# Kernel optimization log

Measured on AMD Instinct MI355X. Metric: run time of the kernel, lower is better.

Reference implementation:

```python
import jax, jax.numpy as jnp
import numpy as np

N_NODES = 100000
N_EDGES = 1600000
IN_CH = 128
HID = 32


def setup_inputs() -> dict:
    key = jax.random.key(0)
    ks = jax.random.split(key, 12)
    x = jax.random.normal(ks[0], (N_NODES, IN_CH), dtype=jnp.float32)
    edge_index = jax.random.randint(ks[1], (2, N_EDGES), 0, N_NODES, dtype=jnp.int64)
    s = lambda fan_in: 1.0 / np.sqrt(fan_in)
    # conv1 MLP: Linear(IN_CH, HID) -> ReLU -> Linear(HID, HID)
    w1a = jax.random.uniform(ks[2], (IN_CH, HID), jnp.float32, -s(IN_CH), s(IN_CH))
    b1a = jax.random.uniform(ks[3], (HID,), jnp.float32, -s(IN_CH), s(IN_CH))
    w1b = jax.random.uniform(ks[4], (HID, HID), jnp.float32, -s(HID), s(HID))
    b1b = jax.random.uniform(ks[5], (HID,), jnp.float32, -s(HID), s(HID))
    # conv2 MLP: Linear(HID, HID) -> ReLU -> Linear(HID, HID)
    w2a = jax.random.uniform(ks[6], (HID, HID), jnp.float32, -s(HID), s(HID))
    b2a = jax.random.uniform(ks[7], (HID,), jnp.float32, -s(HID), s(HID))
    w2b = jax.random.uniform(ks[8], (HID, HID), jnp.float32, -s(HID), s(HID))
    b2b = jax.random.uniform(ks[9], (HID,), jnp.float32, -s(HID), s(HID))
    # conv3 MLP: Linear(HID, 1)
    w3 = jax.random.uniform(ks[10], (HID, 1), jnp.float32, -s(HID), s(HID))
    b3 = jax.random.uniform(ks[11], (1,), jnp.float32, -s(HID), s(HID))
    return {"x": x, "edge_index": edge_index,
            "w1a": w1a, "b1a": b1a, "w1b": w1b, "b1b": b1b,
            "w2a": w2a, "b2a": b2a, "w2b": w2b, "b2b": b2b,
            "w3": w3, "b3": b3}


def _gin_aggregate(x, src, dst):
    # sum of source-node features into destination nodes; eps=0 => add self
    agg = jax.ops.segment_sum(x[src], dst, num_segments=N_NODES)
    return x + agg


def reference(x, edge_index, w1a, b1a, w1b, b1b, w2a, b2a, w2b, b2b, w3, b3):
    src, dst = edge_index[0], edge_index[1]
    # conv1: GINConv with MLP(IN_CH->HID->HID)
    h = _gin_aggregate(x, src, dst)
    h = jax.nn.relu(h @ w1a + b1a) @ w1b + b1b
    # dropout is identity in eval mode
    # conv2
    h = _gin_aggregate(h, src, dst)
    h = jax.nn.relu(h @ w2a + b2a) @ w2b + b2b
    # conv3: MLP is a single Linear(HID, 1)
    h = _gin_aggregate(h, src, dst)
    return h @ w3 + b3
```

## Files before the change

### kernel.cpp

```cpp
#include <hip/hip_runtime.h>

#define NN 100000
#define NE 1600000
#define IC 128
#define HID 32
#define NB 782
#define BCAP 2560
#define EB 4096
#define NBA 391
#define NPJ 782

typedef unsigned short ushort_t;
typedef __attribute__((ext_vector_type(8))) short short8v;
typedef __attribute__((ext_vector_type(4))) float f32x4;

__device__ __forceinline__ ushort_t f2bf(float x) {
    unsigned u = __float_as_uint(x);
    unsigned r = (u + 0x7fffu + ((u >> 16) & 1u)) >> 16;
    return (ushort_t)r;
}
__device__ __forceinline__ float bf2f(ushort_t b) {
    return __uint_as_float(((unsigned)b) << 16);
}

__device__ __forceinline__ int edge_at(const void* ei, int i64f, long long idx) {
    return i64f ? (int)((const long long*)ei)[idx] : ((const int*)ei)[idx];
}

__global__ __launch_bounds__(1024) void setup_kernel(const void* ei, const float* __restrict__ w1a,
                                                     const float* __restrict__ w1b, const float* __restrict__ b1b,
                                                     const float* __restrict__ w2a, const float* __restrict__ w2b,
                                                     const float* __restrict__ b2b, const float* __restrict__ w3,
                                                     int* flag, int* gcursor,
                                                     float* Wc, float* bc1, float* wc2, float* c0,
                                                     ushort_t* Bfrag) {
    int t = threadIdx.x;
    if (blockIdx.x == 1) {
        if (t < NB) gcursor[t] = 0;
        return;
    }
    if (blockIdx.x == 2) {
        if (t < 512) {
            int s = t >> 7, u = (t >> 6) & 1, l = t & 63;
            int krow = s * 32 + (l >> 4) * 8;
            int col = u * 16 + (l & 15);
            #pragma unroll
            for (int j = 0; j < 8; j++)
                Bfrag[t * 8 + j] = f2bf(w1a[(krow + j) * 32 + col]);
        }
        return;
    }
    if (t < 64) {
        const long long* p = (const long long*)ei;
        long long v = p[t];
        unsigned long long bad = __ballot(v < 0 || v >= NN);
        if (t == 0) *flag = (bad == 0ull) ? 1 : 0;
    }
    int k = t >> 5, j = t & 31;
    float acc = 0.f;
    for (int m = 0; m < HID; m++) acc += w1b[k * HID + m] * w2a[m * HID + j];
    Wc[k * HID + j] = acc;
    if (t < 32) {
        float a = 0.f;
        for (int m = 0; m < HID; m++) a += b1b[m] * w2a[m * HID + t];
        bc1[t] = a;
    } else if (t < 64) {
        int kk = t - 32;
        float a = 0.f;
        for (int jj = 0; jj < HID; jj++) a += w2b[kk * HID + jj] * w3[jj];
        wc2[kk] = a;
    } else if (t == 64) {
        float a = 0.f;
        for (int jj = 0; jj < HID; jj++) a += b2b[jj] * w3[jj];
        *c0 = a;
    }
}

__global__ __launch_bounds__(512) void proj_bin_kernel(const float* __restrict__ x,
                                                       const ushort_t* __restrict__ Bfrag,
                                                       ushort_t* __restrict__ y1,
                                                       const void* ei, const int* flag,
                                                       int* gcursor,
                                                       unsigned int* __restrict__ binned) {
    __shared__ int raws[EB];
    __shared__ int rawd[EB];
    __shared__ int hh[NB];
    __shared__ int lcur[NB];
    int t = threadIdx.x;

    if (blockIdx.x < NBA) {
        int bb = blockIdx.x;
        for (int b = t; b < NB; b += 512) hh[b] = 0;
        __syncthreads();
        int i64f = *flag;
        long long ebase = (long long)bb * EB;
        #pragma unroll
        for (int q = 0; q < EB / 512; q++) {
            int i = q * 512 + t;
            long long e = ebase + i;
            int s = 0, d = -1;
            if (e < NE) {
                s = edge_at(ei, i64f, e);
                d = edge_at(ei, i64f, NE + e);
                atomicAdd(&hh[d >> 7], 1);
            }
            raws[i] = s;
            rawd[i] = d;
        }
        __syncthreads();
        for (int b = t; b < NB; b += 512)
            lcur[b] = hh[b] ? atomicAdd(&gcursor[b], hh[b]) : 0;
        __syncthreads();
        #pragma unroll
        for (int q = 0; q < EB / 512; q++) {
            int i = q * 512 + t;
            int d = rawd[i];
            if (d >= 0) {
                int b = d >> 7;
                int pos = atomicAdd(&lcur[b], 1);
                binned[(size_t)b * BCAP + pos] = ((unsigned)raws[i] << 7) | (unsigned)(d & 127);
            }
        }
    } else {
        int pb = blockIdx.x - NBA;
        int wv = t >> 6, l = t & 63;
        int base = pb * 128 + wv * 16;
        int row = l & 15;
        int kg = l >> 4;
        size_t m = (size_t)(base + row);
        if (m >= NN) m = NN - 1;
        const float* xr = x + m * 128 + kg * 8;

        f32x4 acc0 = {0.f, 0.f, 0.f, 0.f};
        f32x4 acc1 = {0.f, 0.f, 0.f, 0.f};
        #pragma unroll
        for (int s = 0; s < 4; s++) {
            float4 xa = *(const float4*)(xr + s * 32);
            float4 xb = *(const float4*)(xr + s * 32 + 4);
            short8v af;
            af[0] = (short)f2bf(xa.x); af[1] = (short)f2bf(xa.y);
            af[2] = (short)f2bf(xa.z); af[3] = (short)f2bf(xa.w);
            af[4] = (short)f2bf(xb.x); af[5] = (short)f2bf(xb.y);
            af[6] = (short)f2bf(xb.z); af[7] = (short)f2bf(xb.w);
            short8v b0 = *(const short8v*)&Bfrag[((s * 2 + 0) * 64 + l) * 8];
            short8v b1 = *(const short8v*)&Bfrag[((s * 2 + 1) * 64 + l) * 8];
            acc0 = __builtin_amdgcn_mfma_f32_16x16x32_bf16(af, b0, acc0, 0, 0, 0);
            acc1 = __builtin_amdgcn_mfma_f32_16x16x32_bf16(af, b1, acc1, 0, 0, 0);
        }
        int col = l & 15;
        #pragma unroll
        for (int r = 0; r < 4; r++) {
            int node = base + kg * 4 + r;
            if (node < NN) {
                y1[(size_t)node * 32 + col]      = f2bf(acc0[r]);
                y1[(size_t)node * 32 + 16 + col] = f2bf(acc1[r]);
            }
        }
    }
}

__global__ __launch_bounds__(512) void bucket_csr_kernel(const unsigned int* __restrict__ binned,
                                                         const int* __restrict__ gcursor,
                                                         int* __restrict__ rowbeg,
                                                         int* __restrict__ rowend,
                                                         int* __restrict__ esrc) {
    __shared__ int cnt[128];
    __shared__ int sc[128];
    __shared__ int cur[128];
    int t = threadIdx.x;
    int b = blockIdx.x;
    int n = gcursor[b];
    int bbase = b * BCAP;
    if (t < 128) cnt[t] = 0;
    __syncthreads();
    for (int p = t; p < n; p += 512)
        atomicAdd(&cnt[binned[bbase + p] & 127], 1);
    __syncthreads();
    if (t < 128) sc[t] = cnt[t];
    __syncthreads();
    for (int off = 1; off < 128; off <<= 1) {
        int a = 0;
        if (t < 128 && t >= off) a = sc[t - off];
        __syncthreads();
        if (t < 128) sc[t] += a;
        __syncthreads();
    }
    if (t < 128) {
        int excl = sc[t] - cnt[t];
        int gn = (b << 7) + t;
        if (gn < NN) { rowbeg[gn] = bbase + excl; rowend[gn] = bbase + excl + cnt[t]; }
        cur[t] = excl;
    }
    __syncthreads();
    for (int p = t; p < n; p += 512) {
        unsigned w = binned[bbase + p];
        int dl = w & 127;
        int pos = bbase + atomicAdd(&cur[dl], 1);
        esrc[pos] = w >> 7;
    }
}

__global__ __launch_bounds__(256) void agg_mlp1_kernel(const ushort_t* __restrict__ y1,
                                                       const int* __restrict__ rowbeg,
                                                       const int* __restrict__ rowend,
                                                       const int* __restrict__ esrc,
                                                       const float* __restrict__ b1a,
                                                       const float* __restrict__ Wc,
                                                       const float* __restrict__ bc1,
                                                       ushort_t* __restrict__ y2) {
    __shared__ float Wl[HID * HID];
    __shared__ float ul[32 * 36];
    int t = threadIdx.x;
    #pragma unroll
    for (int i = 0; i < 4; i++) Wl[i * 256 + t] = Wc[i * 256 + t];

    int g = t >> 3;
    int l = t & 7;
    int n = blockIdx.x * 32 + g;

    int beg = rowbeg[n], end = rowend[n];
    float ax = 0.f, ay = 0.f, az = 0.f, aw = 0.f;
    float bx = 0.f, by = 0.f, bz = 0.f, bw = 0.f;
    float cx = 0.f, cy = 0.f, cz = 0.f, cw = 0.f;
    float dx = 0.f, dy = 0.f, dz = 0.f, dw = 0.f;
    int p = beg;
    for (; p + 4 <= end; p += 4) {
        int s0 = esrc[p], s1 = esrc[p + 1], s2 = esrc[p + 2], s3 = esrc[p + 3];
        ushort4 u0 = *(const ushort4*)&y1[(size_t)s0 * 32 + l * 4];
        ushort4 u1 = *(const ushort4*)&y1[(size_t)s1 * 32 + l * 4];
        ushort4 u2 = *(const ushort4*)&y1[(size_t)s2 * 32 + l * 4];
        ushort4 u3 = *(const ushort4*)&y1[(size_t)s3 * 32 + l * 4];
        ax += bf2f(u0.x); ay += bf2f(u0.y); az += bf2f(u0.z); aw += bf2f(u0.w);
        bx += bf2f(u1.x); by += bf2f(u1.y); bz += bf2f(u1.z); bw += bf2f(u1.w);
        cx += bf2f(u2.x); cy += bf2f(u2.y); cz += bf2f(u2.z); cw += bf2f(u2.w);
        dx += bf2f(u3.x); dy += bf2f(u3.y); dz += bf2f(u3.z); dw += bf2f(u3.w);
    }
    for (; p < end; p++) {
        ushort4 u0 = *(const ushort4*)&y1[(size_t)esrc[p] * 32 + l * 4];
        ax += bf2f(u0.x); ay += bf2f(u0.y); az += bf2f(u0.z); aw += bf2f(u0.w);
    }
    ushort4 us = *(const ushort4*)&y1[(size_t)n * 32 + l * 4];
    float u0 = (ax + bx) + (cx + dx) + bf2f(us.x) + b1a[l * 4 + 0];
    float u1 = (ay + by) + (cy + dy) + bf2f(us.y) + b1a[l * 4 + 1];
    float u2 = (az + bz) + (cz + dz) + bf2f(us.z) + b1a[l * 4 + 2];
    float u3 = (aw + bw) + (cw + dw) + bf2f(us.w) + b1a[l * 4 + 3];
    u0 = u0 > 0.f ? u0 : 0.f;
    u1 = u1 > 0.f ? u1 : 0.f;
    u2 = u2 > 0.f ? u2 : 0.f;
    u3 = u3 > 0.f ? u3 : 0.f;
    *(float4*)&ul[g * 36 + l * 4] = make_float4(u0, u1, u2, u3);
    __syncthreads();

    float4 acc = *(const float4*)&bc1[l * 4];
    #pragma unroll
    for (int k = 0; k < HID; k++) {
        float uk = ul[g * 36 + k];
        float4 wv = *(const float4*)&Wl[k * HID + l * 4];
        acc.x += uk * wv.x; acc.y += uk * wv.y;
        acc.z += uk * wv.z; acc.w += uk * wv.w;
    }
    ushort4 ov;
    ov.x = f2bf(acc.x); ov.y = f2bf(acc.y); ov.z = f2bf(acc.z); ov.w = f2bf(acc.w);
    *(ushort4*)&y2[(size_t)n * 32 + l * 4] = ov;
}

__global__ __launch_bounds__(256) void agg_mlp2_kernel(const ushort_t* __restrict__ y2,
                                                       const int* __restrict__ rowbeg,
                                                       const int* __restrict__ rowend,
                                                       const int* __restrict__ esrc,
                                                       const float* __restrict__ b2a,
                                                       const float* __restrict__ wc2,
                                                       const float* __restrict__ c0,
                                                       float* __restrict__ sbuf) {
    int t = threadIdx.x;
    int g = t >> 3;
    int l = t & 7;
    int n = blockIdx.x * 32 + g;

    int beg = rowbeg[n], end = rowend[n];
    float ax = 0.f, ay = 0.f, az = 0.f, aw = 0.f;
    float bx = 0.f, by = 0.f, bz = 0.f, bw = 0.f;
    float cx = 0.f, cy = 0.f, cz = 0.f, cw = 0.f;
    float dx = 0.f, dy = 0.f, dz = 0.f, dw = 0.f;
    int p = beg;
    for (; p + 4 <= end; p += 4) {
        int s0 = esrc[p], s1 = esrc[p + 1], s2 = esrc[p + 2], s3 = esrc[p + 3];
        ushort4 u0 = *(const ushort4*)&y2[(size_t)s0 * 32 + l * 4];
        ushort4 u1 = *(const ushort4*)&y2[(size_t)s1 * 32 + l * 4];
        ushort4 u2 = *(const ushort4*)&y2[(size_t)s2 * 32 + l * 4];
        ushort4 u3 = *(const ushort4*)&y2[(size_t)s3 * 32 + l * 4];
        ax += bf2f(u0.x); ay += bf2f(u0.y); az += bf2f(u0.z); aw += bf2f(u0.w);
        bx += bf2f(u1.x); by += bf2f(u1.y); bz += bf2f(u1.z); bw += bf2f(u1.w);
        cx += bf2f(u2.x); cy += bf2f(u2.y); cz += bf2f(u2.z); cw += bf2f(u2.w);
        dx += bf2f(u3.x); dy += bf2f(u3.y); dz += bf2f(u3.z); dw += bf2f(u3.w);
    }
    for (; p < end; p++) {
        ushort4 u0 = *(const ushort4*)&y2[(size_t)esrc[p] * 32 + l * 4];
        ax += bf2f(u0.x); ay += bf2f(u0.y); az += bf2f(u0.z); aw += bf2f(u0.w);
    }
    ushort4 us = *(const ushort4*)&y2[(size_t)n * 32 + l * 4];
    float u0 = (ax + bx) + (cx + dx) + bf2f(us.x) + b2a[l * 4 + 0];
    float u1 = (ay + by) + (cy + dy) + bf2f(us.y) + b2a[l * 4 + 1];
    float u2 = (az + bz) + (cz + dz) + bf2f(us.z) + b2a[l * 4 + 2];
    float u3 = (aw + bw) + (cw + dw) + bf2f(us.w) + b2a[l * 4 + 3];
    u0 = u0 > 0.f ? u0 : 0.f;
    u1 = u1 > 0.f ? u1 : 0.f;
    u2 = u2 > 0.f ? u2 : 0.f;
    u3 = u3 > 0.f ? u3 : 0.f;

    float4 w4 = *(const float4*)&wc2[l * 4];
    float s = u0 * w4.x + u1 * w4.y + u2 * w4.z + u3 * w4.w;
    s += __shfl_xor(s, 1);
    s += __shfl_xor(s, 2);
    s += __shfl_xor(s, 4);
    if (l == 0) sbuf[n] = s + *c0;
}

__global__ __launch_bounds__(256) void final_kernel(const float* __restrict__ sbuf,
                                                    const int* __restrict__ rowbeg,
                                                    const int* __restrict__ rowend,
                                                    const int* __restrict__ esrc,
                                                    const float* __restrict__ b3,
                                                    float* __restrict__ out) {
    int n = blockIdx.x * 256 + threadIdx.x;
    if (n >= NN) return;
    float v = sbuf[n] + b3[0];
    int beg = rowbeg[n], end = rowend[n];
    int p = beg;
    for (; p + 4 <= end; p += 4) {
        int s0 = esrc[p], s1 = esrc[p + 1], s2 = esrc[p + 2], s3 = esrc[p + 3];
        float g0 = sbuf[s0], g1 = sbuf[s1], g2 = sbuf[s2], g3 = sbuf[s3];
        v += g0; v += g1; v += g2; v += g3;
    }
    for (; p < end; p++) v += sbuf[esrc[p]];
    out[n] = v;
}

extern "C" void kernel_launch(void* const* d_in, const int* in_sizes, int n_in,
                              void* d_out, int out_size, void* d_ws, size_t ws_size,
                              hipStream_t stream) {
    const float* x   = (const float*)d_in[0];
    const void*  ei  = d_in[1];
    const float* w1a = (const float*)d_in[2];
    const float* b1a = (const float*)d_in[3];
    const float* w1b = (const float*)d_in[4];
    const float* b1b = (const float*)d_in[5];
    const float* w2a = (const float*)d_in[6];
    const float* b2a = (const float*)d_in[7];
    const float* w2b = (const float*)d_in[8];
    const float* b2b = (const float*)d_in[9];
    const float* w3  = (const float*)d_in[10];
    const float* b3  = (const float*)d_in[11];
    float* out = (float*)d_out;

    char* w = (char*)d_ws;
    ushort_t*     y1      = (ushort_t*)(w + 0);
    ushort_t*     y2      = (ushort_t*)(w + 6400000);
    int*          esrc    = (int*)     (w + 12800000);
    int*          rowbeg  = (int*)     (w + 20807680);
    int*          rowend  = (int*)     (w + 21207680);
    float*        sbuf    = (float*)   (w + 21607680);
    int*          gcursor = (int*)     (w + 22007680);
    int*          flag    = (int*)     (w + 22010816);
    float*        Wc      = (float*)   (w + 22010832);
    float*        bc1     = (float*)   (w + 22014928);
    float*        wc2     = (float*)   (w + 22015056);
    float*        c0      = (float*)   (w + 22015184);
    unsigned int* binned  = (unsigned int*)(w + 22015232);
    ushort_t*     Bfrag   = (ushort_t*)(w + 30022912);

    setup_kernel<<<3, 1024, 0, stream>>>(ei, w1a, w1b, b1b, w2a, w2b, b2b, w3,
                                         flag, gcursor, Wc, bc1, wc2, c0, Bfrag);
    proj_bin_kernel<<<NBA + NPJ, 512, 0, stream>>>(x, Bfrag, y1, ei, flag, gcursor, binned);
    bucket_csr_kernel<<<NB, 512, 0, stream>>>(binned, gcursor, rowbeg, rowend, esrc);

    agg_mlp1_kernel<<<NN / 32, 256, 0, stream>>>(y1, rowbeg, rowend, esrc, b1a, Wc, bc1, y2);
    agg_mlp2_kernel<<<NN / 32, 256, 0, stream>>>(y2, rowbeg, rowend, esrc, b2a, wc2, c0, sbuf);

    final_kernel<<<(NN + 255) / 256, 256, 0, stream>>>(sbuf, rowbeg, rowend, esrc, b3, out);
}
```

Measured before the change: 106.3 us.

## Fuse bucket CSR build with first aggregation+MLP kernel using LDS edge list

```diff
diff --git a/kernel.cpp b/kernel.cpp
--- a/kernel.cpp
+++ b/kernel.cpp
@@ -159,21 +159,31 @@
     }
 }
 
-__global__ __launch_bounds__(512) void bucket_csr_kernel(const unsigned int* __restrict__ binned,
-                                                         const int* __restrict__ gcursor,
-                                                         int* __restrict__ rowbeg,
-                                                         int* __restrict__ rowend,
-                                                         int* __restrict__ esrc) {
+__global__ __launch_bounds__(1024) void csr_agg1_kernel(const unsigned int* __restrict__ binned,
+                                                        const int* __restrict__ gcursor,
+                                                        const ushort_t* __restrict__ y1,
+                                                        const float* __restrict__ b1a,
+                                                        const float* __restrict__ Wc,
+                                                        const float* __restrict__ bc1,
+                                                        int* __restrict__ rowbeg,
+                                                        int* __restrict__ rowend,
+                                                        int* __restrict__ esrc,
+                                                        ushort_t* __restrict__ y2) {
     __shared__ int cnt[128];
     __shared__ int sc[128];
     __shared__ int cur[128];
+    __shared__ int esl[BCAP];
+    __shared__ float Wl[HID * HID];
+    __shared__ float ul[128 * 36];
     int t = threadIdx.x;
     int b = blockIdx.x;
-    int n = gcursor[b];
+    int n_edges = gcursor[b];
     int bbase = b * BCAP;
+
+    Wl[t] = Wc[t];
     if (t < 128) cnt[t] = 0;
     __syncthreads();
-    for (int p = t; p < n; p += 512)
+    for (int p = t; p < n_edges; p += 1024)
         atomicAdd(&cnt[binned[bbase + p] & 127], 1);
     __syncthreads();
     if (t < 128) sc[t] = cnt[t];
@@ -187,45 +197,34 @@
     }
     if (t < 128) {
         int excl = sc[t] - cnt[t];
+        cur[t] = excl;
         int gn = (b << 7) + t;
         if (gn < NN) { rowbeg[gn] = bbase + excl; rowend[gn] = bbase + excl + cnt[t]; }
-        cur[t] = excl;
-    }
-    __syncthreads();
-    for (int p = t; p < n; p += 512) {
-        unsigned w = binned[bbase + p];
-        int dl = w & 127;
-        int pos = bbase + atomicAdd(&cur[dl], 1);
-        esrc[pos] = w >> 7;
-    }
-}
-
-__global__ __launch_bounds__(256) void agg_mlp1_kernel(const ushort_t* __restrict__ y1,
-                                                       const int* __restrict__ rowbeg,
-                                                       const int* __restrict__ rowend,
-                                                       const int* __restrict__ esrc,
-                                                       const float* __restrict__ b1a,
-                                                       const float* __restrict__ Wc,
-                                                       const float* __restrict__ bc1,
-                                                       ushort_t* __restrict__ y2) {
-    __shared__ float Wl[HID * HID];
-    __shared__ float ul[32 * 36];
-    int t = threadIdx.x;
-    #pragma unroll
-    for (int i = 0; i < 4; i++) Wl[i * 256 + t] = Wc[i * 256 + t];
+    }
+    __syncthreads();
+    for (int p = t; p < n_edges; p += 1024) {
+        unsigned wv = binned[bbase + p];
+        int dl = wv & 127;
+        int pos = atomicAdd(&cur[dl], 1);
+        int src = (int)(wv >> 7);
+        esl[pos] = src;
+        esrc[bbase + pos] = src;
+    }
+    __syncthreads();
 
     int g = t >> 3;
     int l = t & 7;
-    int n = blockIdx.x * 32 + g;
-
-    int beg = rowbeg[n], end = rowend[n];
+    int gn = (b << 7) + g;
+    int beg = sc[g] - cnt[g];
+    int end = sc[g];
+
     float ax = 0.f, ay = 0.f, az = 0.f, aw = 0.f;
     float bx = 0.f, by = 0.f, bz = 0.f, bw = 0.f;
     float cx = 0.f, cy = 0.f, cz = 0.f, cw = 0.f;
     float dx = 0.f, dy = 0.f, dz = 0.f, dw = 0.f;
     int p = beg;
     for (; p + 4 <= end; p += 4) {
-        int s0 = esrc[p], s1 = esrc[p + 1], s2 = esrc[p + 2], s3 = esrc[p + 3];
+        int s0 = esl[p], s1 = esl[p + 1], s2 = esl[p + 2], s3 = esl[p + 3];
         ushort4 u0 = *(const ushort4*)&y1[(size_t)s0 * 32 + l * 4];
         ushort4 u1 = *(const ushort4*)&y1[(size_t)s1 * 32 + l * 4];
         ushort4 u2 = *(const ushort4*)&y1[(size_t)s2 * 32 + l * 4];
@@ -236,32 +235,35 @@
         dx += bf2f(u3.x); dy += bf2f(u3.y); dz += bf2f(u3.z); dw += bf2f(u3.w);
     }
     for (; p < end; p++) {
-        ushort4 u0 = *(const ushort4*)&y1[(size_t)esrc[p] * 32 + l * 4];
+        ushort4 u0 = *(const ushort4*)&y1[(size_t)esl[p] * 32 + l * 4];
         ax += bf2f(u0.x); ay += bf2f(u0.y); az += bf2f(u0.z); aw += bf2f(u0.w);
     }
-    ushort4 us = *(const ushort4*)&y1[(size_t)n * 32 + l * 4];
-    float u0 = (ax + bx) + (cx + dx) + bf2f(us.x) + b1a[l * 4 + 0];
-    float u1 = (ay + by) + (cy + dy) + bf2f(us.y) + b1a[l * 4 + 1];
-    float u2 = (az + bz) + (cz + dz) + bf2f(us.z) + b1a[l * 4 + 2];
-    float u3 = (aw + bw) + (cw + dw) + bf2f(us.w) + b1a[l * 4 + 3];
-    u0 = u0 > 0.f ? u0 : 0.f;
-    u1 = u1 > 0.f ? u1 : 0.f;
-    u2 = u2 > 0.f ? u2 : 0.f;
-    u3 = u3 > 0.f ? u3 : 0.f;
-    *(float4*)&ul[g * 36 + l * 4] = make_float4(u0, u1, u2, u3);
-    __syncthreads();
-
-    float4 acc = *(const float4*)&bc1[l * 4];
-    #pragma unroll
-    for (int k = 0; k < HID; k++) {
-        float uk = ul[g * 36 + k];
-        float4 wv = *(const float4*)&Wl[k * HID + l * 4];
-        acc.x += uk * wv.x; acc.y += uk * wv.y;
-        acc.z += uk * wv.z; acc.w += uk * wv.w;
-    }
-    ushort4 ov;
-    ov.x = f2bf(acc.x); ov.y = f2bf(acc.y); ov.z = f2bf(acc.z); ov.w = f2bf(acc.w);
-    *(ushort4*)&y2[(size_t)n * 32 + l * 4] = ov;
+    if (gn < NN) {
+        ushort4 us = *(const ushort4*)&y1[(size_t)gn * 32 + l * 4];
+        float u0 = (ax + bx) + (cx + dx) + bf2f(us.x) + b1a[l * 4 + 0];
+        float u1 = (ay + by) + (cy + dy) + bf2f(us.y) + b1a[l * 4 + 1];
+        float u2 = (az + bz) + (cz + dz) + bf2f(us.z) + b1a[l * 4 + 2];
+        float u3 = (aw + bw) + (cw + dw) + bf2f(us.w) + b1a[l * 4 + 3];
+        u0 = u0 > 0.f ? u0 : 0.f;
+        u1 = u1 > 0.f ? u1 : 0.f;
+        u2 = u2 > 0.f ? u2 : 0.f;
+        u3 = u3 > 0.f ? u3 : 0.f;
+        *(float4*)&ul[g * 36 + l * 4] = make_float4(u0, u1, u2, u3);
+    }
+    __syncthreads();
+    if (gn < NN) {
+        float4 acc = *(const float4*)&bc1[l * 4];
+        #pragma unroll
+        for (int k = 0; k < HID; k++) {
+            float uk = ul[g * 36 + k];
+            float4 wv = *(const float4*)&Wl[k * HID + l * 4];
+            acc.x += uk * wv.x; acc.y += uk * wv.y;
+            acc.z += uk * wv.z; acc.w += uk * wv.w;
+        }
+        ushort4 ov;
+        ov.x = f2bf(acc.x); ov.y = f2bf(acc.y); ov.z = f2bf(acc.z); ov.w = f2bf(acc.w);
+        *(ushort4*)&y2[(size_t)gn * 32 + l * 4] = ov;
+    }
 }
 
 __global__ __launch_bounds__(256) void agg_mlp2_kernel(const ushort_t* __restrict__ y2,
@@ -372,9 +374,9 @@
     setup_kernel<<<3, 1024, 0, stream>>>(ei, w1a, w1b, b1b, w2a, w2b, b2b, w3,
                                          flag, gcursor, Wc, bc1, wc2, c0, Bfrag);
     proj_bin_kernel<<<NBA + NPJ, 512, 0, stream>>>(x, Bfrag, y1, ei, flag, gcursor, binned);
-    bucket_csr_kernel<<<NB, 512, 0, stream>>>(binned, gcursor, rowbeg, rowend, esrc);
-
-    agg_mlp1_kernel<<<NN / 32, 256, 0, stream>>>(y1, rowbeg, rowend, esrc, b1a, Wc, bc1, y2);
+
+    csr_agg1_kernel<<<NB, 1024, 0, stream>>>(binned, gcursor, y1, b1a, Wc, bc1,
+                                             rowbeg, rowend, esrc, y2);
     agg_mlp2_kernel<<<NN / 32, 256, 0, stream>>>(y2, rowbeg, rowend, esrc, b2a, wc2, c0, sbuf);
 
     final_kernel<<<(NN + 255) / 256, 256, 0, stream>>>(sbuf, rowbeg, rowend, esrc, b3, out);
```

Measured after the change: 105.3 us. About the same (-1.0%).
